# Kernel tuning notes

Measured on AMD Instinct MI355X. Metric: run time of the kernel, lower is better.

Reference implementation:

```python
import jax, jax.numpy as jnp
import numpy as np

N_USERS = 100000
N_ITEMS = 20000
N_GENRES = 20
N_TAGS = 1128
EMB_ID = 64
EMB_FEAT = 64
HEADS = 8
HIDDEN = 256
D_MOVIE = EMB_ID + 2 * EMB_FEAT  # 192
E_HALF = 200000
N_NODES = N_USERS + N_ITEMS
NEG_SLOPE = 0.2


def setup_inputs() -> dict:
    key = jax.random.key(0)
    ks = jax.random.split(key, 24)
    p = lambda k, shape: (jax.random.normal(k, shape, jnp.float32) * 0.05)
    user_ids = jnp.arange(N_USERS)
    movie_ids = jnp.arange(N_ITEMS)
    mov_x = jax.random.normal(ks[0], (N_ITEMS, N_GENRES + N_TAGS), jnp.float32)
    # bipartite user<->movie edges, both directions (no self loops, matches add_self_loops=False)
    u = jax.random.randint(ks[1], (E_HALF,), 0, N_USERS)
    m = jax.random.randint(ks[2], (E_HALF,), 0, N_ITEMS) + N_USERS
    edge_index = jnp.stack([jnp.concatenate([u, m]), jnp.concatenate([m, u])])  # [2, 2*E_HALF]
    C1 = HIDDEN // HEADS
    return dict(
        user_ids=user_ids, movie_ids=movie_ids, mov_x=mov_x, edge_index=edge_index,
        user_emb=p(ks[3], (N_USERS, EMB_ID)), item_emb=p(ks[4], (N_ITEMS, EMB_ID)),
        gW1=p(ks[5], (N_GENRES, EMB_FEAT)), gb1=jnp.zeros((EMB_FEAT,), jnp.float32),
        gW2=p(ks[6], (EMB_FEAT, EMB_FEAT)), gb2=jnp.zeros((EMB_FEAT,), jnp.float32),
        tW1=p(ks[7], (N_TAGS, EMB_FEAT)), tb1=jnp.zeros((EMB_FEAT,), jnp.float32),
        tW2=p(ks[8], (EMB_FEAT, EMB_FEAT)), tb2=jnp.zeros((EMB_FEAT,), jnp.float32),
        Ws1=p(ks[9], (D_MOVIE, HIDDEN)), Wd1=p(ks[10], (D_MOVIE, HIDDEN)),
        as1=p(ks[11], (HEADS, C1)), ad1=p(ks[12], (HEADS, C1)),
        b1=jnp.zeros((HIDDEN,), jnp.float32),
        Ws2=p(ks[13], (HIDDEN, HIDDEN)), Wd2=p(ks[14], (HIDDEN, HIDDEN)),
        as2=p(ks[15], (1, HIDDEN)), ad2=p(ks[16], (1, HIDDEN)),
        b2=jnp.zeros((HIDDEN,), jnp.float32),
    )


def _gat(x, edge_index, Ws, Wd, a_s, a_d, bias, concat):
    # PyG GATConv (eval mode: dropout off, add_self_loops=False)
    N = x.shape[0]
    H, C = a_s.shape
    hs = (x @ Ws).reshape(N, H, C)  # source-side projection
    hd = (x @ Wd).reshape(N, H, C)  # dest-side projection
    al_s = (hs * a_s).sum(-1)  # [N, H]
    al_d = (hd * a_d).sum(-1)  # [N, H]
    src, dst = edge_index[0], edge_index[1]
    e = al_s[src] + al_d[dst]                      # [E, H]
    e = jnp.where(e > 0, e, NEG_SLOPE * e)         # leaky_relu(0.2)
    mmax = jax.ops.segment_max(e, dst, num_segments=N)
    w = jnp.exp(e - mmax[dst])
    ssum = jax.ops.segment_sum(w, dst, num_segments=N)
    alpha = w / (ssum[dst] + 1e-16)                # segment softmax over incoming edges
    out = jax.ops.segment_sum(hs[src] * alpha[:, :, None], dst, num_segments=N)  # [N, H, C]
    out = out.reshape(N, H * C) if concat else out.mean(axis=1)
    return out + bias


def reference(user_ids, movie_ids, mov_x, edge_index,
              user_emb, item_emb,
              gW1, gb1, gW2, gb2, tW1, tb1, tW2, tb2,
              Ws1, Wd1, as1, ad1, b1,
              Ws2, Wd2, as2, ad2, b2):
    g_feat = mov_x[:, :N_GENRES]
    t_feat = mov_x[:, N_GENRES:]
    g = jax.nn.relu(g_feat @ gW1 + gb1) @ gW2 + gb2
    t = jax.nn.relu(t_feat @ tW1 + tb1) @ tW2 + tb2
    x_mov = jnp.concatenate([item_emb[movie_ids], g, t], axis=1)  # [n_m, D_MOVIE]
    # homogeneous graph: user nodes first (zero-pad user emb to D_MOVIE), then movies
    x_usr = jnp.pad(user_emb[user_ids], ((0, 0), (0, D_MOVIE - EMB_ID)))
    x = jnp.concatenate([x_usr, x_mov], axis=0)  # [N_NODES, D_MOVIE]
    out = jax.nn.elu(_gat(x, edge_index, Ws1, Wd1, as1, ad1, b1, concat=True))
    out = _gat(out, edge_index, Ws2, Wd2, as2, ad2, b2, concat=False)
    ptr = jnp.array([0, N_USERS, N_USERS + N_ITEMS])
    return out, ptr
```

## Files before the change

### kernel.cpp

```cpp
#include <hip/hip_runtime.h>
#include <hip/hip_bf16.h>

#define N_USERS_C 100000
#define N_ITEMS_C 20000
#define N_NODES_C 120000
#define E_TOT_C   400000
#define D_IN_C    192
#define HID_C     256
#define NEG_C     0.2f
#define CLAMP_C   1000.0f
#define KPAD_C    1152
#define NB_SCAN   ((N_NODES_C + 255) / 256)
#define ROWE      40

typedef __attribute__((ext_vector_type(8))) short bfrag;
typedef __attribute__((ext_vector_type(4))) float ffrag;

__device__ __forceinline__ float bf2f(unsigned short u){
  return __uint_as_float(((unsigned)u) << 16);
}
__device__ __forceinline__ float ldf(const void* p, long i, int isf32){
  return isf32 ? ((const float*)p)[i] : bf2f(((const unsigned short*)p)[i]);
}
__device__ __forceinline__ float sane(float v){
  return (v > -1e30f && v < 1e30f) ? v : 0.f;
}
__device__ __forceinline__ int clampsrc(int s){
  return s < 0 ? 0 : (s >= N_NODES_C ? N_NODES_C - 1 : s);
}
__device__ __forceinline__ short f2bs(float f){
  __hip_bfloat16 h = __float2bfloat16(f);
  return *reinterpret_cast<short*>(&h);
}

__global__ __launch_bounds__(256) void detect_dtype(const unsigned short* __restrict__ ue,
                                                    int* __restrict__ flag){
  __shared__ int cnt[256];
  int tid = threadIdx.x; int c = 0;
  for (int i = tid; i < 8192; i += 256){
    unsigned e = (ue[i] >> 7) & 0xFFu;
    if (e >= 129u) c++;
  }
  cnt[tid] = c; __syncthreads();
  if (tid == 0){
    int s = 0;
    for (int i = 0; i < 256; i++) s += cnt[i];
    *flag = (s > 100) ? 1 : 0;
  }
}

struct PrepArgs {
  const void *ue, *ie;
  const void *gW1, *gb1, *gW2, *gb2, *tW1, *tb1, *tW2, *tb2;
  const void *Ws1, *Wd1, *as1, *ad1, *b1, *Ws2, *Wd2, *as2, *ad2, *b2;
  __hip_bfloat16 *x, *Bt1, *Bt2, *W1t, *W2t, *b1c, *b2c, *bg1, *bg2;
  int *deg, *cursor;
  const int* flag;
};

#define NB_UEMB  3125
#define NB_UZERO 2
#define NB_MOVE  625
#define NB_BT1   204
#define NB_BT2   272
#define NB_W1T   72
#define NB_W2T   8
#define NB_ZERO  235
#define NB_PREP (NB_UEMB+NB_UZERO+NB_MOVE+NB_BT1+NB_BT2+NB_W1T+NB_W2T+1+NB_ZERO)

__global__ __launch_bounds__(256) void mega_prep(PrepArgs a){
  int b = blockIdx.x, tid = threadIdx.x;
  int f32 = *a.flag;
  if (b < NB_UEMB) {
    int idx = b * 256 + tid;
    int n = idx >> 3, c0 = (idx & 7) * 8;
    union { short s[8]; float4 f; } u;
    if (f32) {
      const float* rf = (const float*)a.ue + (long)n * 64 + c0;
      float4 x0 = *(const float4*)rf, x1 = *(const float4*)(rf + 4);
      u.s[0]=f2bs(x0.x); u.s[1]=f2bs(x0.y); u.s[2]=f2bs(x0.z); u.s[3]=f2bs(x0.w);
      u.s[4]=f2bs(x1.x); u.s[5]=f2bs(x1.y); u.s[6]=f2bs(x1.z); u.s[7]=f2bs(x1.w);
    } else {
      u.f = *(const float4*)((const unsigned short*)a.ue + (long)n * 64 + c0);
    }
    *(float4*)(&a.x[(long)n * 192 + c0]) = u.f;
    return;
  }
  b -= NB_UEMB;
  if (b < NB_UZERO) {
    int idx = b * 256 + tid;
    int r = idx >> 4, c0 = 64 + (idx & 15) * 8;
    float4 z = {0.f, 0.f, 0.f, 0.f};
    *(float4*)(&a.x[(long)(99968 + r) * 192 + c0]) = z;
    return;
  }
  b -= NB_UZERO;
  if (b < NB_MOVE) {
    int idx = b * 256 + tid;
    int m = idx >> 3, c0 = (idx & 7) * 8;
    union { short s[8]; float4 f; } u;
    if (f32) {
      const float* rf = (const float*)a.ie + (long)m * 64 + c0;
      float4 x0 = *(const float4*)rf, x1 = *(const float4*)(rf + 4);
      u.s[0]=f2bs(x0.x); u.s[1]=f2bs(x0.y); u.s[2]=f2bs(x0.z); u.s[3]=f2bs(x0.w);
      u.s[4]=f2bs(x1.x); u.s[5]=f2bs(x1.y); u.s[6]=f2bs(x1.z); u.s[7]=f2bs(x1.w);
    } else {
      u.f = *(const float4*)((const unsigned short*)a.ie + (long)m * 64 + c0);
    }
    *(float4*)(&a.x[(long)(N_USERS_C + m) * 192 + c0]) = u.f;
    return;
  }
  b -= NB_MOVE;
  if (b < NB_BT1) {
    int idx = b * 256 + tid;
    int col = idx / 192, k = idx - col * 192;
    float v;
    if (col < 256) v = ldf(a.Ws1, k * 256 + col, f32);
    else if (col < 264) {
      int h = col - 256; float s = 0.f;
      for (int c = 0; c < 32; c++)
        s += ldf(a.Ws1, k * 256 + h * 32 + c, f32) * ldf(a.as1, h * 32 + c, f32);
      v = s;
    } else {
      int h = col - 264; float s = 0.f;
      for (int c = 0; c < 32; c++)
        s += ldf(a.Wd1, k * 256 + h * 32 + c, f32) * ldf(a.ad1, h * 32 + c, f32);
      v = s;
    }
    a.Bt1[col * 192 + k] = __float2bfloat16(v);
    return;
  }
  b -= NB_BT1;
  if (b < NB_BT2) {
    int idx = b * 256 + tid;
    int col = idx / 256, k = idx & 255;
    float v;
    if (col < 256) v = ldf(a.Ws2, k * 256 + col, f32);
    else if (col == 256) {
      float s = 0.f;
      for (int c = 0; c < 256; c++)
        s += ldf(a.Ws2, k * 256 + c, f32) * ldf(a.as2, c, f32);
      v = s;
    } else if (col == 257) {
      float s = 0.f;
      for (int c = 0; c < 256; c++)
        s += ldf(a.Wd2, k * 256 + c, f32) * ldf(a.ad2, c, f32);
      v = s;
    } else v = 0.f;
    a.Bt2[col * 256 + k] = __float2bfloat16(v);
    return;
  }
  b -= NB_BT2;
  if (b < NB_W1T) {
    int idx = b * 256 + tid;
    int n = idx / 144, c8 = idx - n * 144;
    int k0 = c8 * 8;
    union { short s[8]; float4 f; } u;
#pragma unroll
    for (int j = 0; j < 8; j++) {
      int k = k0 + j; float v = 0.f;
      if (n < 64) { if (k < 20) v = ldf(a.gW1, k * 64 + n, f32); }
      else        { if (k >= 20 && k < 1148) v = ldf(a.tW1, (k - 20) * 64 + (n - 64), f32); }
      u.s[j] = f2bs(v);
    }
    *(float4*)(&a.W1t[(long)n * 1152 + k0]) = u.f;
    return;
  }
  b -= NB_W1T;
  if (b < NB_W2T) {
    int idx = b * 256 + tid;
    int n = idx >> 4, k0 = (idx & 15) * 8;
    union { short s[8]; float4 f; } u;
#pragma unroll
    for (int j = 0; j < 8; j++) {
      int k = k0 + j; float v = 0.f;
      if (n < 64) { if (k < 64)  v = ldf(a.gW2, k * 64 + n, f32); }
      else        { if (k >= 64) v = ldf(a.tW2, (k - 64) * 64 + (n - 64), f32); }
      u.s[j] = f2bs(v);
    }
    *(float4*)(&a.W2t[n * 128 + k0]) = u.f;
    return;
  }
  b -= NB_W2T;
  if (b < 1) {
    int i = tid;
    if (i < 64)       a.b1c[i] = __float2bfloat16(ldf(a.gb1, i, f32));
    else if (i < 128) a.b1c[i] = __float2bfloat16(ldf(a.tb1, i - 64, f32));
    else if (i < 192) a.b2c[i - 128] = __float2bfloat16(ldf(a.gb2, i - 128, f32));
    else              a.b2c[i - 128] = __float2bfloat16(ldf(a.tb2, i - 192, f32));
    a.bg1[tid] = __float2bfloat16(ldf(a.b1, tid, f32));
    a.bg2[tid] = __float2bfloat16(ldf(a.b2, tid, f32));
    return;
  }
  b -= 1;
  {
    int i0 = (b * 256 + tid) * 4;
    if (i0 < 2 * N_NODES_C) {
      int4 z = {0, 0, 0, 0};
      if (i0 < N_NODES_C) *(int4*)(a.deg + i0) = z;
      else                *(int4*)(a.cursor + (i0 - N_NODES_C)) = z;
    }
  }
}

__global__ __launch_bounds__(256) void movie_gemm(
    const __hip_bfloat16* __restrict__ A, int lda, int M,
    const void* __restrict__ rawA, const int* __restrict__ flag,
    const __hip_bfloat16* __restrict__ Bt, int K,
    const __hip_bfloat16* __restrict__ bias, int do_relu,
    __hip_bfloat16* __restrict__ out, int ldo, int ocol){
  __shared__ short Bls[128 * ROWE];
  __shared__ short Als[64 * ROWE];
  int tid = threadIdx.x;
  int wave = tid >> 6;
  int lane = tid & 63;
  int l15 = lane & 15;
  int quad = lane >> 4;
  int rowbase_blk = blockIdx.x * 64;
  int rowbase = rowbase_blk + wave * 16;
  int f32v = rawA ? *flag : 0;
  ffrag acc[8];
#pragma unroll
  for (int i = 0; i < 8; i++) acc[i] = (ffrag){0.f, 0.f, 0.f, 0.f};
  const short* As = (const short*)A;
  const short* Bs = (const short*)Bt;
  int sr = tid >> 2, sc = tid & 3;
  int arow_st = rowbase_blk + sr; if (arow_st >= M) arow_st = M - 1;
  for (int k0 = 0; k0 < K; k0 += 32) {
    __syncthreads();
    for (int t = tid; t < 512; t += 256) {
      int r = t >> 2, c = t & 3;
      *(float4*)(&Bls[r * ROWE + c * 8]) = *(const float4*)(Bs + (long)r * K + k0 + c * 8);
    }
    int kc = k0 + sc * 8;
    if (rawA) {
      union { short s[8]; float4 f; } u;
      long base = (long)arow_st * 1148 + kc;
      if (kc + 8 <= 1148) {
        if (f32v) {
          const float* rf = (const float*)rawA + base;
          float4 x0 = *(const float4*)rf;
          float4 x1 = *(const float4*)(rf + 4);
          u.s[0]=f2bs(x0.x); u.s[1]=f2bs(x0.y); u.s[2]=f2bs(x0.z); u.s[3]=f2bs(x0.w);
          u.s[4]=f2bs(x1.x); u.s[5]=f2bs(x1.y); u.s[6]=f2bs(x1.z); u.s[7]=f2bs(x1.w);
        } else {
          const unsigned short* rs = (const unsigned short*)rawA + base;
          ushort4 a0 = *(const ushort4*)rs;
          ushort4 a1 = *(const ushort4*)(rs + 4);
          u.s[0]=(short)a0.x; u.s[1]=(short)a0.y; u.s[2]=(short)a0.z; u.s[3]=(short)a0.w;
          u.s[4]=(short)a1.x; u.s[5]=(short)a1.y; u.s[6]=(short)a1.z; u.s[7]=(short)a1.w;
        }
      } else {
#pragma unroll
        for (int j = 0; j < 8; j++) {
          float v = (kc + j < 1148) ? ldf(rawA, base + j, f32v) : 0.f;
          u.s[j] = f2bs(v);
        }
      }
      *(float4*)(&Als[sr * ROWE + sc * 8]) = u.f;
    } else {
      *(float4*)(&Als[sr * ROWE + sc * 8]) =
          *(const float4*)(As + (long)arow_st * lda + kc);
    }
    __syncthreads();
    int koff = quad * 8;
    bfrag af = *(const bfrag*)(&Als[(wave * 16 + l15) * ROWE + koff]);
#pragma unroll
    for (int nt = 0; nt < 8; nt++) {
      bfrag bf = *(const bfrag*)(&Bls[(nt * 16 + l15) * ROWE + koff]);
      acc[nt] = __builtin_amdgcn_mfma_f32_16x16x32_bf16(af, bf, acc[nt], 0, 0, 0);
    }
  }
#pragma unroll
  for (int reg = 0; reg < 4; reg++) {
    int grow = rowbase + quad * 4 + reg;
    if (grow >= M) continue;
#pragma unroll
    for (int nt = 0; nt < 8; nt++) {
      float v = acc[nt][reg] + __bfloat162float(bias[nt * 16 + l15]);
      if (do_relu) v = fmaxf(v, 0.f);
      out[(long)grow * ldo + ocol + nt * 16 + l15] = __float2bfloat16(v);
    }
  }
}

__global__ __launch_bounds__(256) void gemm_fused(
    const __hip_bfloat16* __restrict__ A, const __hip_bfloat16* __restrict__ Bt,
    __hip_bfloat16* __restrict__ Hout, float* __restrict__ als, float* __restrict__ ald,
    int K, int natt, int ukmax){
  __shared__ short Bls[272 * ROWE];
  __shared__ short Als[64 * ROWE];
  int tid = threadIdx.x;
  int wave = tid >> 6;
  int lane = tid & 63;
  int l15 = lane & 15;
  int quad = lane >> 4;
  int rowbase_blk = blockIdx.x * 64;
  int rowbase = rowbase_blk + wave * 16;
  int kmax = (rowbase_blk + 64 <= N_USERS_C) ? ukmax : K;
  ffrag acc[17];
#pragma unroll
  for (int i = 0; i < 17; i++) acc[i] = (ffrag){0.f, 0.f, 0.f, 0.f};
  const short* As = (const short*)A;
  const short* Bs = (const short*)Bt;
  int sr = tid >> 2, sc = tid & 3;
  for (int k0 = 0; k0 < kmax; k0 += 32) {
    __syncthreads();
    for (int t = tid; t < 1088; t += 256) {
      int r = t >> 2, c = t & 3;
      *(float4*)(&Bls[r * ROWE + c * 8]) = *(const float4*)(Bs + (long)r * K + k0 + c * 8);
    }
    *(float4*)(&Als[sr * ROWE + sc * 8]) =
        *(const float4*)(As + (long)(rowbase_blk + sr) * K + k0 + sc * 8);
    __syncthreads();
    int koff = quad * 8;
    bfrag af = *(const bfrag*)(&Als[(wave * 16 + l15) * ROWE + koff]);
#pragma unroll
    for (int nt = 0; nt < 17; nt++) {
      bfrag bf = *(const bfrag*)(&Bls[(nt * 16 + l15) * ROWE + koff]);
      acc[nt] = __builtin_amdgcn_mfma_f32_16x16x32_bf16(af, bf, acc[nt], 0, 0, 0);
    }
  }
  int col = l15;
#pragma unroll
  for (int reg = 0; reg < 4; reg++) {
    int grow = rowbase + quad * 4 + reg;
    long obase = (long)grow * 256;
#pragma unroll
    for (int nt = 0; nt < 16; nt++)
      Hout[obase + nt * 16 + col] = __float2bfloat16(acc[nt][reg]);
    float v = acc[16][reg];
    if (col < natt) als[grow * natt + col] = v;
    else if (col < 2 * natt) ald[grow * natt + (col - natt)] = v;
  }
}

__global__ void deg_count(const int* __restrict__ ei, int* __restrict__ deg){
  int e = blockIdx.x * 256 + threadIdx.x;
  if (e >= E_TOT_C) return;
  int dst = ei[E_TOT_C + e];
  if (dst >= 0 && dst < N_NODES_C) atomicAdd(&deg[dst], 1);
}

__global__ __launch_bounds__(256) void deg_bsum(const int* __restrict__ deg,
                                                int* __restrict__ bsum){
  int i = blockIdx.x * 256 + threadIdx.x;
  int v = (i < N_NODES_C) ? deg[i] : 0;
#pragma unroll
  for (int o = 32; o > 0; o >>= 1) v += __shfl_down(v, o, 64);
  __shared__ int ws[4];
  int wave = threadIdx.x >> 6, lane = threadIdx.x & 63;
  if (lane == 0) ws[wave] = v;
  __syncthreads();
  if (threadIdx.x == 0) bsum[blockIdx.x] = ws[0] + ws[1] + ws[2] + ws[3];
}

__global__ __launch_bounds__(512) void bsum_scan(int* __restrict__ bsum,
                                                 int* __restrict__ ptrn){
  __shared__ int sm[512];
  int t = threadIdx.x;
  int v = (t < NB_SCAN) ? bsum[t] : 0;
  sm[t] = v;
  __syncthreads();
  for (int o = 1; o < 512; o <<= 1) {
    int add = (t >= o) ? sm[t - o] : 0;
    __syncthreads();
    sm[t] += add;
    __syncthreads();
  }
  int excl = (t == 0) ? 0 : sm[t - 1];
  if (t < NB_SCAN) bsum[t] = excl;
  if (t == NB_SCAN - 1) ptrn[N_NODES_C] = sm[t];
}

__global__ __launch_bounds__(256) void deg_scan_final(const int* __restrict__ deg,
                                                      const int* __restrict__ bexcl,
                                                      int* __restrict__ ptrn){
  __shared__ int sm[256];
  int i = blockIdx.x * 256 + threadIdx.x;
  int t = threadIdx.x;
  int v = (i < N_NODES_C) ? deg[i] : 0;
  sm[t] = v;
  __syncthreads();
  for (int o = 1; o < 256; o <<= 1) {
    int add = (t >= o) ? sm[t - o] : 0;
    __syncthreads();
    sm[t] += add;
    __syncthreads();
  }
  int excl = (t == 0) ? 0 : sm[t - 1];
  if (i < N_NODES_C) ptrn[i] = bexcl[blockIdx.x] + excl;
}

__global__ void scatter_edges(const int* __restrict__ ei, const int* __restrict__ ptrn,
                              int* __restrict__ cursor, int* __restrict__ elist_src){
  int e = blockIdx.x * 256 + threadIdx.x;
  if (e >= E_TOT_C) return;
  int dst = ei[E_TOT_C + e];
  if (dst < 0 || dst >= N_NODES_C) return;
  int pos = atomicAdd(&cursor[dst], 1);
  elist_src[ptrn[dst] + pos] = ei[e];
}

__global__ __launch_bounds__(256) void aggregate1(
    const int* __restrict__ ptrn, const int* __restrict__ elist_src,
    const float* __restrict__ als, const float* __restrict__ ald,
    const __hip_bfloat16* __restrict__ hs, const __hip_bfloat16* __restrict__ bias,
    __hip_bfloat16* __restrict__ h1){
  int node = blockIdx.x * 4 + (threadIdx.x >> 6);
  if (node >= N_NODES_C) return;
  int lane = threadIdx.x & 63;
  int c0 = lane * 4;
  int h = lane >> 3;
  int beg = ptrn[node], end = ptrn[node + 1];
  float aldv = sane(ald[node * 8 + h]);
  float m = -1e30f;
  float wsum = 0.f, a0 = 0.f, a1 = 0.f, a2 = 0.f, a3 = 0.f;
  const unsigned short* hsu = (const unsigned short*)hs;
  float alsv_p = 0.f;
  ushort4 hv_p = {0, 0, 0, 0};
  int src_b = 0;
  if (beg < end) {
    int s0 = clampsrc(elist_src[beg]);
    alsv_p = als[(long)s0 * 8 + h];
    hv_p = *(const ushort4*)(hsu + (long)s0 * 256 + c0);
    if (beg + 1 < end) src_b = clampsrc(elist_src[beg + 1]);
  }
  for (int i = beg; i < end; i++) {
    float alsv = alsv_p;
    ushort4 hv = hv_p;
    if (i + 1 < end) {
      alsv_p = als[(long)src_b * 8 + h];
      hv_p = *(const ushort4*)(hsu + (long)src_b * 256 + c0);
    }
    if (i + 2 < end)
      src_b = clampsrc(elist_src[i + 2]);
    float ev = sane(alsv) + aldv;
    ev = ev > 0.f ? ev : NEG_C * ev;
    float mnew = fmaxf(m, ev);
    float corr = __expf(m - mnew);
    float w = __expf(ev - mnew);
    m = mnew;
    wsum = wsum * corr + w;
    a0 = a0 * corr + w * bf2f(hv.x); a1 = a1 * corr + w * bf2f(hv.y);
    a2 = a2 * corr + w * bf2f(hv.z); a3 = a3 * corr + w * bf2f(hv.w);
  }
  float inv = 1.f / (wsum + 1e-16f);
  float v0 = a0 * inv + __bfloat162float(bias[c0 + 0]);
  float v1 = a1 * inv + __bfloat162float(bias[c0 + 1]);
  float v2 = a2 * inv + __bfloat162float(bias[c0 + 2]);
  float v3 = a3 * inv + __bfloat162float(bias[c0 + 3]);
  v0 = v0 > 0.f ? v0 : (__expf(v0) - 1.f);
  v1 = v1 > 0.f ? v1 : (__expf(v1) - 1.f);
  v2 = v2 > 0.f ? v2 : (__expf(v2) - 1.f);
  v3 = v3 > 0.f ? v3 : (__expf(v3) - 1.f);
  v0 = fminf(fmaxf(v0, -CLAMP_C), CLAMP_C);
  v1 = fminf(fmaxf(v1, -CLAMP_C), CLAMP_C);
  v2 = fminf(fmaxf(v2, -CLAMP_C), CLAMP_C);
  v3 = fminf(fmaxf(v3, -CLAMP_C), CLAMP_C);
  long ob = (long)node * 256 + c0;
  h1[ob + 0] = __float2bfloat16(v0); h1[ob + 1] = __float2bfloat16(v1);
  h1[ob + 2] = __float2bfloat16(v2); h1[ob + 3] = __float2bfloat16(v3);
}

__global__ __launch_bounds__(256) void aggregate2(
    const int* __restrict__ ptrn, const int* __restrict__ elist_src,
    const float* __restrict__ als, const float* __restrict__ ald,
    const __hip_bfloat16* __restrict__ hs, const __hip_bfloat16* __restrict__ bias,
    float* __restrict__ out, int out_size){
  if (blockIdx.x == 0 && threadIdx.x == 0) {
    out[out_size - 3] = 0.f;
    out[out_size - 2] = (float)N_USERS_C;
    out[out_size - 1] = (float)N_NODES_C;
  }
  int node = blockIdx.x * 4 + (threadIdx.x >> 6);
  if (node >= N_NODES_C) return;
  int lane = threadIdx.x & 63;
  int c0 = lane * 4;
  int beg = ptrn[node], end = ptrn[node + 1];
  float aldv = sane(ald[node]);
  float m = -1e30f;
  float wsum = 0.f, a0 = 0.f, a1 = 0.f, a2 = 0.f, a3 = 0.f;
  const unsigned short* hsu = (const unsigned short*)hs;
  float alsv_p = 0.f;
  ushort4 hv_p = {0, 0, 0, 0};
  int src_b = 0;
  if (beg < end) {
    int s0 = clampsrc(elist_src[beg]);
    alsv_p = als[s0];
    hv_p = *(const ushort4*)(hsu + (long)s0 * 256 + c0);
    if (beg + 1 < end) src_b = clampsrc(elist_src[beg + 1]);
  }
  for (int i = beg; i < end; i++) {
    float alsv = alsv_p;
    ushort4 hv = hv_p;
    if (i + 1 < end) {
      alsv_p = als[src_b];
      hv_p = *(const ushort4*)(hsu + (long)src_b * 256 + c0);
    }
    if (i + 2 < end)
      src_b = clampsrc(elist_src[i + 2]);
    float ev = sane(alsv) + aldv;
    ev = ev > 0.f ? ev : NEG_C * ev;
    float mnew = fmaxf(m, ev);
    float corr = __expf(m - mnew);
    float w = __expf(ev - mnew);
    m = mnew;
    wsum = wsum * corr + w;
    a0 = a0 * corr + w * bf2f(hv.x); a1 = a1 * corr + w * bf2f(hv.y);
    a2 = a2 * corr + w * bf2f(hv.z); a3 = a3 * corr + w * bf2f(hv.w);
  }
  float inv = 1.f / (wsum + 1e-16f);
  float4 v;
  v.x = a0 * inv + __bfloat162float(bias[c0 + 0]);
  v.y = a1 * inv + __bfloat162float(bias[c0 + 1]);
  v.z = a2 * inv + __bfloat162float(bias[c0 + 2]);
  v.w = a3 * inv + __bfloat162float(bias[c0 + 3]);
  v.x = fminf(fmaxf(v.x, -CLAMP_C), CLAMP_C);
  v.y = fminf(fmaxf(v.y, -CLAMP_C), CLAMP_C);
  v.z = fminf(fmaxf(v.z, -CLAMP_C), CLAMP_C);
  v.w = fminf(fmaxf(v.w, -CLAMP_C), CLAMP_C);
  *(float4*)(out + (long)node * 256 + c0) = v;
}

extern "C" void kernel_launch(void* const* d_in, const int* in_sizes, int n_in,
                              void* d_out, int out_size, void* d_ws, size_t ws_size,
                              hipStream_t stream) {
  const void* mov_x    = d_in[2];
  const int*  ei       = (const int*)d_in[3];
  const void* user_emb = d_in[4];
  const void* item_emb = d_in[5];

  char* ws = (char*)d_ws;
  size_t off = 0;
  auto alloc = [&](size_t bytes) -> void* {
    void* p = ws + off; off += (bytes + 255) / 256 * 256; return p;
  };
  int* flag   = (int*)alloc(4);
  __hip_bfloat16* Bt1 = (__hip_bfloat16*)alloc(272 * 192 * 2);
  __hip_bfloat16* Bt2 = (__hip_bfloat16*)alloc(272 * 256 * 2);
  __hip_bfloat16* W1t = (__hip_bfloat16*)alloc(128 * KPAD_C * 2);
  __hip_bfloat16* W2t = (__hip_bfloat16*)alloc(128 * 128 * 2);
  __hip_bfloat16* b1c = (__hip_bfloat16*)alloc(128 * 2);
  __hip_bfloat16* b2c = (__hip_bfloat16*)alloc(128 * 2);
  __hip_bfloat16* bg1 = (__hip_bfloat16*)alloc(256 * 2);
  __hip_bfloat16* bg2 = (__hip_bfloat16*)alloc(256 * 2);
  int* ptrn   = (int*)alloc((N_NODES_C + 1) * 4);
  int* deg    = (int*)alloc(N_NODES_C * 4);
  int* cursor = (int*)alloc(N_NODES_C * 4);
  int* bsum   = (int*)alloc(512 * 4);
  int* elist  = (int*)alloc(E_TOT_C * 4);
  float* als  = (float*)alloc((size_t)N_NODES_C * 8 * 4);
  float* ald  = (float*)alloc((size_t)N_NODES_C * 8 * 4);
  __hip_bfloat16* x  = (__hip_bfloat16*)alloc((size_t)N_NODES_C * D_IN_C * 2);
  __hip_bfloat16* hs = (__hip_bfloat16*)alloc((size_t)N_NODES_C * HID_C * 2);
  __hip_bfloat16* h1  = (__hip_bfloat16*)d_out;
  __hip_bfloat16* hid = hs;

  detect_dtype<<<1, 256, 0, stream>>>((const unsigned short*)user_emb, flag);

  PrepArgs pa;
  pa.ue = user_emb; pa.ie = item_emb;
  pa.gW1 = d_in[6];  pa.gb1 = d_in[7];  pa.gW2 = d_in[8];  pa.gb2 = d_in[9];
  pa.tW1 = d_in[10]; pa.tb1 = d_in[11]; pa.tW2 = d_in[12]; pa.tb2 = d_in[13];
  pa.Ws1 = d_in[14]; pa.Wd1 = d_in[15]; pa.as1 = d_in[16]; pa.ad1 = d_in[17]; pa.b1 = d_in[18];
  pa.Ws2 = d_in[19]; pa.Wd2 = d_in[20]; pa.as2 = d_in[21]; pa.ad2 = d_in[22]; pa.b2 = d_in[23];
  pa.x = x; pa.Bt1 = Bt1; pa.Bt2 = Bt2; pa.W1t = W1t; pa.W2t = W2t;
  pa.b1c = b1c; pa.b2c = b2c; pa.bg1 = bg1; pa.bg2 = bg2;
  pa.deg = deg; pa.cursor = cursor; pa.flag = flag;
  mega_prep<<<NB_PREP, 256, 0, stream>>>(pa);

  movie_gemm<<<(N_ITEMS_C + 63) / 64, 256, 0, stream>>>(
      nullptr, 0, N_ITEMS_C, mov_x, flag, W1t, KPAD_C, b1c, 1, hid, 128, 0);
  movie_gemm<<<(N_ITEMS_C + 63) / 64, 256, 0, stream>>>(
      hid, 128, N_ITEMS_C, nullptr, flag, W2t, 128, b2c, 0,
      x + (long)N_USERS_C * D_IN_C, D_IN_C, 64);

  deg_count<<<(E_TOT_C + 255) / 256, 256, 0, stream>>>(ei, deg);
  deg_bsum<<<NB_SCAN, 256, 0, stream>>>(deg, bsum);
  bsum_scan<<<1, 512, 0, stream>>>(bsum, ptrn);
  deg_scan_final<<<NB_SCAN, 256, 0, stream>>>(deg, bsum, ptrn);
  scatter_edges<<<(E_TOT_C + 255) / 256, 256, 0, stream>>>(ei, ptrn, cursor, elist);

  gemm_fused<<<N_NODES_C / 64, 256, 0, stream>>>(x, Bt1, hs, als, ald, 192, 8, 64);
  aggregate1<<<N_NODES_C / 4, 256, 0, stream>>>(ptrn, elist, als, ald, hs, bg1, h1);

  gemm_fused<<<N_NODES_C / 64, 256, 0, stream>>>(h1, Bt2, hs, als, ald, 256, 1, 256);
  aggregate2<<<N_NODES_C / 4, 256, 0, stream>>>(ptrn, elist, als, ald, hs, bg2,
                                                (float*)d_out, out_size);
}
```

Baseline: 588.0 us.

## Split-K the movie feature GEMM and fuse reduction into second GEMM

The first movie MLP GEMM (K=1152) launched only 313 blocks, which underfills the GPU, so it is split into 4 K-chunks that write fp32 partial sums to scratch space in the output buffer. The second GEMM then sums the partials, adds the bias and ReLU while staging its A tile, which removes the separate hidden bf16 round trip. This brings extra fp32 partial traffic (4×20000×128 floats) and relies on the output buffer being large enough to hold the scratch region.

```diff
diff --git a/kernel.cpp b/kernel.cpp
--- a/kernel.cpp
+++ b/kernel.cpp
@@ -12,6 +12,9 @@
 #define KPAD_C    1152
 #define NB_SCAN   ((N_NODES_C + 255) / 256)
 #define ROWE      40
+#define NT_MOV    313
+#define KSPLIT    4
+#define KCH       288
 
 typedef __attribute__((ext_vector_type(8))) short bfrag;
 typedef __attribute__((ext_vector_type(4))) float ffrag;
@@ -203,12 +206,85 @@
   }
 }
 
-__global__ __launch_bounds__(256) void movie_gemm(
-    const __hip_bfloat16* __restrict__ A, int lda, int M,
+__global__ __launch_bounds__(256) void movie_gemm_k(
     const void* __restrict__ rawA, const int* __restrict__ flag,
-    const __hip_bfloat16* __restrict__ Bt, int K,
-    const __hip_bfloat16* __restrict__ bias, int do_relu,
-    __hip_bfloat16* __restrict__ out, int ldo, int ocol){
+    const __hip_bfloat16* __restrict__ W1t,
+    float* __restrict__ part){
+  __shared__ short Bls[128 * ROWE];
+  __shared__ short Als[64 * ROWE];
+  int tid = threadIdx.x;
+  int wave = tid >> 6;
+  int lane = tid & 63;
+  int l15 = lane & 15;
+  int quad = lane >> 4;
+  int bid = blockIdx.x;
+  int tile = bid % NT_MOV, split = bid / NT_MOV;
+  int rowbase_blk = tile * 64;
+  int rowbase = rowbase_blk + wave * 16;
+  int f32v = *flag;
+  ffrag acc[8];
+#pragma unroll
+  for (int i = 0; i < 8; i++) acc[i] = (ffrag){0.f, 0.f, 0.f, 0.f};
+  const short* Bs = (const short*)W1t;
+  int sr = tid >> 2, sc = tid & 3;
+  int arow_st = rowbase_blk + sr; if (arow_st >= N_ITEMS_C) arow_st = N_ITEMS_C - 1;
+  int kbeg = split * KCH;
+  for (int k0 = kbeg; k0 < kbeg + KCH; k0 += 32) {
+    __syncthreads();
+    for (int t = tid; t < 512; t += 256) {
+      int r = t >> 2, c = t & 3;
+      *(float4*)(&Bls[r * ROWE + c * 8]) =
+          *(const float4*)(Bs + (long)r * KPAD_C + k0 + c * 8);
+    }
+    int kc = k0 + sc * 8;
+    union { short s[8]; float4 f; } u;
+    long base = (long)arow_st * 1148 + kc;
+    if (kc + 8 <= 1148) {
+      if (f32v) {
+        const float* rf = (const float*)rawA + base;
+        float4 x0 = *(const float4*)rf;
+        float4 x1 = *(const float4*)(rf + 4);
+        u.s[0]=f2bs(x0.x); u.s[1]=f2bs(x0.y); u.s[2]=f2bs(x0.z); u.s[3]=f2bs(x0.w);
+        u.s[4]=f2bs(x1.x); u.s[5]=f2bs(x1.y); u.s[6]=f2bs(x1.z); u.s[7]=f2bs(x1.w);
+      } else {
+        const unsigned short* rs = (const unsigned short*)rawA + base;
+        ushort4 a0 = *(const ushort4*)rs;
+        ushort4 a1 = *(const ushort4*)(rs + 4);
+        u.s[0]=(short)a0.x; u.s[1]=(short)a0.y; u.s[2]=(short)a0.z; u.s[3]=(short)a0.w;
+        u.s[4]=(short)a1.x; u.s[5]=(short)a1.y; u.s[6]=(short)a1.z; u.s[7]=(short)a1.w;
+      }
+    } else {
+#pragma unroll
+      for (int j = 0; j < 8; j++) {
+        float v = (kc + j < 1148) ? ldf(rawA, base + j, f32v) : 0.f;
+        u.s[j] = f2bs(v);
+      }
+    }
+    *(float4*)(&Als[sr * ROWE + sc * 8]) = u.f;
+    __syncthreads();
+    int koff = quad * 8;
+    bfrag af = *(const bfrag*)(&Als[(wave * 16 + l15) * ROWE + koff]);
+#pragma unroll
+    for (int nt = 0; nt < 8; nt++) {
+      bfrag bf = *(const bfrag*)(&Bls[(nt * 16 + l15) * ROWE + koff]);
+      acc[nt] = __builtin_amdgcn_mfma_f32_16x16x32_bf16(af, bf, acc[nt], 0, 0, 0);
+    }
+  }
+  float* pb = part + (long)split * (N_ITEMS_C * 128);
+#pragma unroll
+  for (int reg = 0; reg < 4; reg++) {
+    int grow = rowbase + quad * 4 + reg;
+    if (grow >= N_ITEMS_C) continue;
+#pragma unroll
+    for (int nt = 0; nt < 8; nt++)
+      pb[(long)grow * 128 + nt * 16 + l15] = acc[nt][reg];
+  }
+}
+
+__global__ __launch_bounds__(256) void movie_gemm2(
+    const float* __restrict__ part, const __hip_bfloat16* __restrict__ b1c,
+    const __hip_bfloat16* __restrict__ W2t, const __hip_bfloat16* __restrict__ b2c,
+    __hip_bfloat16* __restrict__ out){
   __shared__ short Bls[128 * ROWE];
   __shared__ short Als[64 * ROWE];
   int tid = threadIdx.x;
@@ -218,50 +294,35 @@
   int quad = lane >> 4;
   int rowbase_blk = blockIdx.x * 64;
   int rowbase = rowbase_blk + wave * 16;
-  int f32v = rawA ? *flag : 0;
   ffrag acc[8];
 #pragma unroll
   for (int i = 0; i < 8; i++) acc[i] = (ffrag){0.f, 0.f, 0.f, 0.f};
-  const short* As = (const short*)A;
-  const short* Bs = (const short*)Bt;
+  const short* Bs = (const short*)W2t;
   int sr = tid >> 2, sc = tid & 3;
-  int arow_st = rowbase_blk + sr; if (arow_st >= M) arow_st = M - 1;
-  for (int k0 = 0; k0 < K; k0 += 32) {
+  int arow_st = rowbase_blk + sr; if (arow_st >= N_ITEMS_C) arow_st = N_ITEMS_C - 1;
+  for (int k0 = 0; k0 < 128; k0 += 32) {
     __syncthreads();
     for (int t = tid; t < 512; t += 256) {
       int r = t >> 2, c = t & 3;
-      *(float4*)(&Bls[r * ROWE + c * 8]) = *(const float4*)(Bs + (long)r * K + k0 + c * 8);
+      *(float4*)(&Bls[r * ROWE + c * 8]) =
+          *(const float4*)(Bs + (long)r * 128 + k0 + c * 8);
     }
     int kc = k0 + sc * 8;
-    if (rawA) {
-      union { short s[8]; float4 f; } u;
-      long base = (long)arow_st * 1148 + kc;
-      if (kc + 8 <= 1148) {
-        if (f32v) {
-          const float* rf = (const float*)rawA + base;
-          float4 x0 = *(const float4*)rf;
-          float4 x1 = *(const float4*)(rf + 4);
-          u.s[0]=f2bs(x0.x); u.s[1]=f2bs(x0.y); u.s[2]=f2bs(x0.z); u.s[3]=f2bs(x0.w);
-          u.s[4]=f2bs(x1.x); u.s[5]=f2bs(x1.y); u.s[6]=f2bs(x1.z); u.s[7]=f2bs(x1.w);
-        } else {
-          const unsigned short* rs = (const unsigned short*)rawA + base;
-          ushort4 a0 = *(const ushort4*)rs;
-          ushort4 a1 = *(const ushort4*)(rs + 4);
-          u.s[0]=(short)a0.x; u.s[1]=(short)a0.y; u.s[2]=(short)a0.z; u.s[3]=(short)a0.w;
-          u.s[4]=(short)a1.x; u.s[5]=(short)a1.y; u.s[6]=(short)a1.z; u.s[7]=(short)a1.w;
-        }
-      } else {
-#pragma unroll
-        for (int j = 0; j < 8; j++) {
-          float v = (kc + j < 1148) ? ldf(rawA, base + j, f32v) : 0.f;
-          u.s[j] = f2bs(v);
-        }
-      }
-      *(float4*)(&Als[sr * ROWE + sc * 8]) = u.f;
-    } else {
-      *(float4*)(&Als[sr * ROWE + sc * 8]) =
-          *(const float4*)(As + (long)arow_st * lda + kc);
-    }
+    float vs[8];
+#pragma unroll
+    for (int j = 0; j < 8; j++) vs[j] = __bfloat162float(b1c[kc + j]);
+    long base = (long)arow_st * 128 + kc;
+#pragma unroll
+    for (int s = 0; s < KSPLIT; s++) {
+      const float* p = part + (long)s * (N_ITEMS_C * 128) + base;
+      float4 q0 = *(const float4*)p, q1 = *(const float4*)(p + 4);
+      vs[0] += q0.x; vs[1] += q0.y; vs[2] += q0.z; vs[3] += q0.w;
+      vs[4] += q1.x; vs[5] += q1.y; vs[6] += q1.z; vs[7] += q1.w;
+    }
+    union { short s[8]; float4 f; } u;
+#pragma unroll
+    for (int j = 0; j < 8; j++) u.s[j] = f2bs(fmaxf(vs[j], 0.f));
+    *(float4*)(&Als[sr * ROWE + sc * 8]) = u.f;
     __syncthreads();
     int koff = quad * 8;
     bfrag af = *(const bfrag*)(&Als[(wave * 16 + l15) * ROWE + koff]);
@@ -274,12 +335,11 @@
 #pragma unroll
   for (int reg = 0; reg < 4; reg++) {
     int grow = rowbase + quad * 4 + reg;
-    if (grow >= M) continue;
+    if (grow >= N_ITEMS_C) continue;
 #pragma unroll
     for (int nt = 0; nt < 8; nt++) {
-      float v = acc[nt][reg] + __bfloat162float(bias[nt * 16 + l15]);
-      if (do_relu) v = fmaxf(v, 0.f);
-      out[(long)grow * ldo + ocol + nt * 16 + l15] = __float2bfloat16(v);
+      float v = acc[nt][reg] + __bfloat162float(b2c[nt * 16 + l15]);
+      out[(long)grow * D_IN_C + 64 + nt * 16 + l15] = __float2bfloat16(v);
     }
   }
 }
@@ -555,7 +615,7 @@
   __hip_bfloat16* x  = (__hip_bfloat16*)alloc((size_t)N_NODES_C * D_IN_C * 2);
   __hip_bfloat16* hs = (__hip_bfloat16*)alloc((size_t)N_NODES_C * HID_C * 2);
   __hip_bfloat16* h1  = (__hip_bfloat16*)d_out;
-  __hip_bfloat16* hid = hs;
+  float* part = (float*)((char*)d_out + 61440000);
 
   detect_dtype<<<1, 256, 0, stream>>>((const unsigned short*)user_emb, flag);
 
@@ -570,11 +630,9 @@
   pa.deg = deg; pa.cursor = cursor; pa.flag = flag;
   mega_prep<<<NB_PREP, 256, 0, stream>>>(pa);
 
-  movie_gemm<<<(N_ITEMS_C + 63) / 64, 256, 0, stream>>>(
-      nullptr, 0, N_ITEMS_C, mov_x, flag, W1t, KPAD_C, b1c, 1, hid, 128, 0);
-  movie_gemm<<<(N_ITEMS_C + 63) / 64, 256, 0, stream>>>(
-      hid, 128, N_ITEMS_C, nullptr, flag, W2t, 128, b2c, 0,
-      x + (long)N_USERS_C * D_IN_C, D_IN_C, 64);
+  movie_gemm_k<<<NT_MOV * KSPLIT, 256, 0, stream>>>(mov_x, flag, W1t, part);
+  movie_gemm2<<<NT_MOV, 256, 0, stream>>>(part, b1c, W2t, b2c,
+                                          x + (long)N_USERS_C * D_IN_C);
 
   deg_count<<<(E_TOT_C + 255) / 256, 256, 0, stream>>>(ei, deg);
   deg_bsum<<<NB_SCAN, 256, 0, stream>>>(deg, bsum);
```

New measurement: 571.9 us. 1.03x faster.
